# Kernel tuning notes

Hardware: AMD Instinct MI355X
Metric: run time of the kernel (lower is better)

Reference implementation:

```python
import jax, jax.numpy as jnp
import numpy as np

EMBED_DIM = 1024
NUM_HEADS = 16
HEAD_DIM = EMBED_DIM // NUM_HEADS
B, S = 4, 1024
EPS = 1e-5
NEG = -1e9


def layer_norm(h, gamma, beta):
    mu = jnp.mean(h, axis=-1, keepdims=True)
    var = jnp.mean(jnp.square(h - mu), axis=-1, keepdims=True)
    return (h - mu) * jax.lax.rsqrt(var + EPS) * gamma + beta


def setup_inputs() -> dict:
    key = jax.random.key(0)
    ks = jax.random.split(key, 8)
    scale = 1.0 / np.sqrt(EMBED_DIM)
    x = jax.random.normal(ks[0], (B, S, EMBED_DIM), dtype=jnp.float32)
    mask = jax.random.randint(ks[1], (B, S, S), 0, 2).astype(jnp.bool_)
    Wq = jax.random.uniform(ks[2], (EMBED_DIM, EMBED_DIM), jnp.float32, -scale, scale)
    bq = jax.random.uniform(ks[3], (EMBED_DIM,), jnp.float32, -scale, scale)
    Wk = jax.random.uniform(ks[4], (EMBED_DIM, EMBED_DIM), jnp.float32, -scale, scale)
    bk = jax.random.uniform(ks[5], (EMBED_DIM,), jnp.float32, -scale, scale)
    gq = jnp.ones((EMBED_DIM,), jnp.float32)
    bq_n = jnp.zeros((EMBED_DIM,), jnp.float32)
    gk = jnp.ones((EMBED_DIM,), jnp.float32)
    bk_n = jnp.zeros((EMBED_DIM,), jnp.float32)
    return {"x": x, "mask": mask, "Wq": Wq, "bq": bq, "Wk": Wk, "bk": bk,
            "gq": gq, "bq_n": bq_n, "gk": gk, "bk_n": bk_n}


def reference(x, mask, Wq, bq, Wk, bk, gq, bq_n, gk, bk_n):
    b, s, _ = x.shape
    # proj -> LayerNorm -> ReLU, split heads: [B,S,H,D]
    Q = jax.nn.relu(layer_norm(x @ Wq + bq, gq, bq_n)).reshape(b, s, NUM_HEADS, HEAD_DIM)
    K = jax.nn.relu(layer_norm(x @ Wk + bk, gk, bk_n)).reshape(b, s, NUM_HEADS, HEAD_DIM)
    # scores [B,H,S,S]
    scores = jnp.einsum('bqhd,bkhd->bhqk', Q, K) / np.sqrt(HEAD_DIM).astype(np.float32)
    # symmetric masking: mask applied along keys, then (via transpose trick) along queries
    m = (mask | jnp.swapaxes(mask, -1, -2))[:, None, :, :]
    scores = jnp.where(m, NEG, scores)
    attn = jax.nn.softmax(scores, axis=-1)
    return attn.mean(axis=1)  # [B,S,S]
```

## Files before the change

### kernel.cpp

```cpp
#include <hip/hip_runtime.h>
#include <hip/hip_bf16.h>

#define B_ 4
#define S_ 1024
#define E_ 1024
#define H_ 16
#define D_ 64

typedef __attribute__((ext_vector_type(8))) short short8;
typedef __attribute__((ext_vector_type(4))) float f32x4;

static __device__ __forceinline__ unsigned short f2bf(float x) {
  unsigned int u = __float_as_uint(x);
  unsigned int r = u + 0x7fffu + ((u >> 16) & 1u);
  return (unsigned short)(r >> 16);
}
static __device__ __forceinline__ float bf2f(unsigned short b) {
  return __uint_as_float((unsigned int)b << 16);
}

#define GL2LDS16(g, l)                                                            \
  __builtin_amdgcn_global_load_lds(                                               \
      (const __attribute__((address_space(1))) unsigned int*)(g),                 \
      (__attribute__((address_space(3))) unsigned int*)(l), 16, 0, 0)

__global__ __launch_bounds__(256) void mask_sym_kernel(const int* __restrict__ mask,
                                                       unsigned char* __restrict__ msym) {
  const int blk = blockIdx.x;
  const int b = blk >> 10;
  const int rest = blk & 1023;
  const int i0 = (rest >> 5) << 5;
  const int j0 = (rest & 31) << 5;
  __shared__ int T[32][33];
  const int tid = threadIdx.x;
  const int ii = tid >> 3;
  const int jj4 = (tid & 7) << 2;
  const size_t bO = (size_t)b * S_ * S_;
  const int4 m2 = *(const int4*)&mask[bO + (size_t)(j0 + ii) * S_ + i0 + jj4];
  T[ii][jj4 + 0] = m2.x; T[ii][jj4 + 1] = m2.y; T[ii][jj4 + 2] = m2.z; T[ii][jj4 + 3] = m2.w;
  __syncthreads();
  const int4 m1 = *(const int4*)&mask[bO + (size_t)(i0 + ii) * S_ + j0 + jj4];
  uchar4 o;
  o.x = ((m1.x != 0) || (T[jj4 + 0][ii] != 0)) ? 1 : 0;
  o.y = ((m1.y != 0) || (T[jj4 + 1][ii] != 0)) ? 1 : 0;
  o.z = ((m1.z != 0) || (T[jj4 + 2][ii] != 0)) ? 1 : 0;
  o.w = ((m1.w != 0) || (T[jj4 + 3][ii] != 0)) ? 1 : 0;
  *(uchar4*)&msym[bO + (size_t)(i0 + ii) * S_ + j0 + jj4] = o;
}

__global__ __launch_bounds__(256) void cvt_x_kernel(const float* __restrict__ x,
                                                    unsigned short* __restrict__ o) {
  const size_t i = ((size_t)blockIdx.x * 256 + threadIdx.x) * 8;
  const float4 a = *(const float4*)(x + i);
  const float4 b = *(const float4*)(x + i + 4);
  const ushort4 p0 = {f2bf(a.x), f2bf(a.y), f2bf(a.z), f2bf(a.w)};
  const ushort4 p1 = {f2bf(b.x), f2bf(b.y), f2bf(b.z), f2bf(b.w)};
  *(ushort4*)(o + i) = p0;
  *(ushort4*)(o + i + 4) = p1;
}

__global__ __launch_bounds__(256) void wt_kernel(const float* __restrict__ Wq,
                                                 const float* __restrict__ Wk,
                                                 unsigned short* __restrict__ Wt) {
  const int blk = blockIdx.x;
  const int mat = blk >> 10;
  const int kt = (blk >> 5) & 31, ntb = blk & 31;
  const float* W = mat ? Wk : Wq;
  __shared__ unsigned short T[32][36];
  const int tid = threadIdx.x;
  const int r = tid >> 3, c4 = (tid & 7) << 2;
  const float4 v = *(const float4*)&W[(size_t)(kt * 32 + r) * 1024 + ntb * 32 + c4];
  T[r][c4 + 0] = f2bf(v.x); T[r][c4 + 1] = f2bf(v.y);
  T[r][c4 + 2] = f2bf(v.z); T[r][c4 + 3] = f2bf(v.w);
  __syncthreads();
  const ushort4 o = {T[c4 + 0][r], T[c4 + 1][r], T[c4 + 2][r], T[c4 + 3][r]};
  *(ushort4*)&Wt[(size_t)(mat * 1024 + ntb * 32 + r) * 1024 + kt * 32 + c4] = o;
}

__global__ __launch_bounds__(256) void gemm_mfma_kernel(const unsigned short* __restrict__ Abf,
                                                        const unsigned short* __restrict__ Wt,
                                                        unsigned short* __restrict__ P,
                                                        int nstride) {
  __shared__ __align__(16) unsigned short As[128 * 32];
  __shared__ __align__(16) unsigned short Bs[128 * 32];
  const int tid = threadIdx.x;
  const int m0 = (blockIdx.x & 31) << 7;
  const int n0 = (blockIdx.x >> 5) << 7;
  const int wave = tid >> 6, lane = tid & 63;
  const int ln15 = lane & 15, rg = lane >> 4;
  const int wm = (wave & 1) << 6;
  const int wn = (wave >> 1) << 6;
  const int sr = tid >> 2;
  const int sc = (tid & 3) << 3;
  const unsigned short* gA = Abf + (size_t)(m0 + sr) * 1024 + sc;
  const unsigned short* gB = Wt + (size_t)(n0 + sr) * 1024 + sc;
  unsigned short* lA = As + tid * 8;
  unsigned short* lB = Bs + tid * 8;
  f32x4 acc[4][4];
#pragma unroll
  for (int i = 0; i < 4; ++i)
#pragma unroll
    for (int j = 0; j < 4; ++j) acc[i][j] = (f32x4){0.0f, 0.0f, 0.0f, 0.0f};

  const unsigned short* pa = As + (wm + ln15) * 32 + rg * 8;
  const unsigned short* pb = Bs + (wn + ln15) * 32 + rg * 8;
  for (int k0 = 0; k0 < E_; k0 += 32) {
    GL2LDS16(gA + k0, lA);
    GL2LDS16(gA + k0 + (size_t)64 * 1024, lA + 2048);
    GL2LDS16(gB + k0, lB);
    GL2LDS16(gB + k0 + (size_t)64 * 1024, lB + 2048);
    __syncthreads();
    short8 af[4], bfr[4];
#pragma unroll
    for (int i = 0; i < 4; ++i) af[i] = *(const short8*)(pa + i * 16 * 32);
#pragma unroll
    for (int j = 0; j < 4; ++j) bfr[j] = *(const short8*)(pb + j * 16 * 32);
#pragma unroll
    for (int i = 0; i < 4; ++i)
#pragma unroll
      for (int j = 0; j < 4; ++j)
        acc[i][j] = __builtin_amdgcn_mfma_f32_16x16x32_bf16(af[i], bfr[j], acc[i][j], 0, 0, 0);
    __syncthreads();
  }
#pragma unroll
  for (int i = 0; i < 4; ++i)
#pragma unroll
    for (int j = 0; j < 4; ++j)
#pragma unroll
      for (int r = 0; r < 4; ++r) {
        const int row = m0 + wm + i * 16 + rg * 4 + r;
        const int col = n0 + wn + j * 16 + ln15;
        P[(size_t)row * nstride + col] = f2bf(acc[i][j][r]);
      }
}

__global__ __launch_bounds__(256) void ln_relu_bf_kernel(const unsigned short* __restrict__ P,
                                                         int rowstride, int coloff,
                                                         const float* __restrict__ bias,
                                                         const float* __restrict__ gamma,
                                                         const float* __restrict__ beta,
                                                         unsigned short* __restrict__ obf) {
  const int row = blockIdx.x;
  const int b = row >> 10, s = row & 1023;
  const unsigned short* p = P + (size_t)row * rowstride + coloff;
  const int tid = threadIdx.x;
  const ushort4 pv = *(const ushort4*)(p + tid * 4);
  float4 v = {bf2f(pv.x), bf2f(pv.y), bf2f(pv.z), bf2f(pv.w)};
  const float4 bb = ((const float4*)bias)[tid];
  v.x += bb.x; v.y += bb.y; v.z += bb.z; v.w += bb.w;
  float sum = v.x + v.y + v.z + v.w;
  float s2 = v.x * v.x + v.y * v.y + v.z * v.z + v.w * v.w;
#pragma unroll
  for (int off = 32; off >= 1; off >>= 1) {
    sum += __shfl_xor(sum, off);
    s2 += __shfl_xor(s2, off);
  }
  __shared__ float red[2][4];
  const int wave = tid >> 6, lane = tid & 63;
  if (lane == 0) { red[0][wave] = sum; red[1][wave] = s2; }
  __syncthreads();
  sum = red[0][0] + red[0][1] + red[0][2] + red[0][3];
  s2 = red[1][0] + red[1][1] + red[1][2] + red[1][3];
  const float mu = sum * (1.0f / E_);
  const float var = s2 * (1.0f / E_) - mu * mu;
  const float r = rsqrtf(var + 1e-5f);
  const float4 g = ((const float4*)gamma)[tid];
  const float4 bt = ((const float4*)beta)[tid];
  const float o0 = fmaxf((v.x - mu) * r * g.x + bt.x, 0.0f);
  const float o1 = fmaxf((v.y - mu) * r * g.y + bt.y, 0.0f);
  const float o2 = fmaxf((v.z - mu) * r * g.z + bt.z, 0.0f);
  const float o3 = fmaxf((v.w - mu) * r * g.w + bt.w, 0.0f);
  const int h = tid >> 4;
  const int d = (tid & 15) << 2;
  const ushort4 ob = {f2bf(o0), f2bf(o1), f2bf(o2), f2bf(o3)};
  *(ushort4*)&obf[((size_t)(b * H_ + h) * S_ + s) * D_ + d] = ob;
}

__global__ __launch_bounds__(1024, 4) void attn4_kernel(const unsigned short* __restrict__ Qbf,
                                                        const unsigned short* __restrict__ Kbf,
                                                        const unsigned char* __restrict__ msym,
                                                        float* __restrict__ out) {
  __shared__ __align__(16) float outAcc[16][1028];
  __shared__ __align__(16) float l_lds[16][4][16];
  __shared__ __align__(16) float linv_lds[4][16];
  const int tid = threadIdx.x;
  const int wave = tid >> 6, lane = tid & 63;
  const int ln15 = lane & 15, rg = lane >> 4;
  const int blk = blockIdx.x;
  const int b = blk & 3;
  const int q0 = (blk >> 2) << 4;
  const int k0 = wave << 6;

  unsigned int mbits = 0;
#pragma unroll
  for (int jt = 0; jt < 4; ++jt)
#pragma unroll
    for (int r = 0; r < 4; ++r)
      mbits |= (msym[((size_t)b * S_ + q0 + rg * 4 + r) * S_ + k0 + jt * 16 + ln15] ? 1u : 0u)
               << (jt * 4 + r);

  const size_t bbase = (size_t)b * H_ * S_ * D_;
  const size_t qoff = (size_t)(q0 + ln15) * D_ + rg * 8;
  const size_t koff = (size_t)(k0 + ln15) * D_ + rg * 8;

  float o[4][4] = {};
#pragma unroll 1
  for (int c = 0; c < 4; ++c) {
    unsigned int epack[4][4][2];
#pragma unroll
    for (int hh = 0; hh < 4; ++hh) {
      const size_t hbase = bbase + (size_t)(c * 4 + hh) * S_ * D_;
      const unsigned short* qp = Qbf + hbase + qoff;
      const short8 a0 = *(const short8*)qp;
      const short8 a1 = *(const short8*)(qp + 32);
      const unsigned short* kp = Kbf + hbase + koff;
      float la[4] = {0.0f, 0.0f, 0.0f, 0.0f};
#pragma unroll
      for (int jt = 0; jt < 4; ++jt) {
        const unsigned short* kpj = kp + (size_t)jt * (16 * D_);
        const short8 b0 = *(const short8*)kpj;
        const short8 b1 = *(const short8*)(kpj + 32);
        f32x4 cc = {0.0f, 0.0f, 0.0f, 0.0f};
        cc = __builtin_amdgcn_mfma_f32_16x16x32_bf16(a0, b0, cc, 0, 0, 0);
        cc = __builtin_amdgcn_mfma_f32_16x16x32_bf16(a1, b1, cc, 0, 0, 0);
        float e[4];
#pragma unroll
        for (int r = 0; r < 4; ++r) {
          const float s = fminf(cc[r] * 0.125f, 80.0f);
          e[r] = ((mbits >> (jt * 4 + r)) & 1u) ? 0.0f : __expf(s);
          la[r] += e[r];
        }
        epack[hh][jt][0] = (unsigned)f2bf(e[0]) | ((unsigned)f2bf(e[1]) << 16);
        epack[hh][jt][1] = (unsigned)f2bf(e[2]) | ((unsigned)f2bf(e[3]) << 16);
      }
#pragma unroll
      for (int r = 0; r < 4; ++r) {
        float lv = la[r];
        lv += __shfl_xor(lv, 1);
        lv += __shfl_xor(lv, 2);
        lv += __shfl_xor(lv, 4);
        lv += __shfl_xor(lv, 8);
        la[r] = lv;
      }
      if (ln15 == 0) {
        const float4 lw = {la[0], la[1], la[2], la[3]};
        *(float4*)&l_lds[wave][hh][rg * 4] = lw;
      }
    }
    __syncthreads();
    if (tid < 64) {
      const int hh = tid >> 4, q = tid & 15;
      float s = 0.0f;
#pragma unroll
      for (int w = 0; w < 16; ++w) s += l_lds[w][hh][q];
      linv_lds[hh][q] = 0.0625f / s;
    }
    __syncthreads();
#pragma unroll
    for (int hh = 0; hh < 4; ++hh) {
      const float4 li4 = *(const float4*)&linv_lds[hh][rg * 4];
#pragma unroll
      for (int jt = 0; jt < 4; ++jt) {
        const unsigned u0 = epack[hh][jt][0], u1 = epack[hh][jt][1];
        o[jt][0] += __uint_as_float(u0 << 16) * li4.x;
        o[jt][1] += __uint_as_float(u0 & 0xFFFF0000u) * li4.y;
        o[jt][2] += __uint_as_float(u1 << 16) * li4.z;
        o[jt][3] += __uint_as_float(u1 & 0xFFFF0000u) * li4.w;
      }
    }
  }
#pragma unroll
  for (int jt = 0; jt < 4; ++jt)
#pragma unroll
    for (int r = 0; r < 4; ++r)
      outAcc[rg * 4 + r][k0 + jt * 16 + ln15] = o[jt][r];
  __syncthreads();
  {
    const int row = tid >> 6, c0 = (tid & 63) << 4;
    float* dst = out + ((size_t)b * S_ + q0 + row) * S_ + c0;
    const float* srcA = &outAcc[row][c0];
#pragma unroll
    for (int i = 0; i < 4; ++i)
      *(float4*)(dst + i * 4) = *(const float4*)(srcA + i * 4);
  }
}

extern "C" void kernel_launch(void* const* d_in, const int* in_sizes, int n_in,
                              void* d_out, int out_size, void* d_ws, size_t ws_size,
                              hipStream_t stream) {
  const float* x = (const float*)d_in[0];
  const int* mask = (const int*)d_in[1];
  const float* Wq = (const float*)d_in[2];
  const float* bq = (const float*)d_in[3];
  const float* Wk = (const float*)d_in[4];
  const float* bk = (const float*)d_in[5];
  const float* gq = (const float*)d_in[6];
  const float* bq_n = (const float*)d_in[7];
  const float* gk = (const float*)d_in[8];
  const float* bk_n = (const float*)d_in[9];
  float* out = (float*)d_out;

  char* ws = (char*)d_ws;
  const size_t MB = 1024 * 1024;

  if (ws_size >= 40 * MB) {
    unsigned short* P2 = (unsigned short*)ws;
    unsigned short* xbf = (unsigned short*)(ws + 16 * MB);
    unsigned short* Kbf = (unsigned short*)(ws + 16 * MB);
    unsigned short* Wt = (unsigned short*)(ws + 24 * MB);
    unsigned short* Qbf = (unsigned short*)(ws + 28 * MB);
    unsigned char* msym = (unsigned char*)(ws + 36 * MB);

    mask_sym_kernel<<<4096, 256, 0, stream>>>(mask, msym);
    cvt_x_kernel<<<2048, 256, 0, stream>>>(x, xbf);
    wt_kernel<<<2048, 256, 0, stream>>>(Wq, Wk, Wt);
    gemm_mfma_kernel<<<512, 256, 0, stream>>>(xbf, Wt, P2, 2048);
    ln_relu_bf_kernel<<<4096, 256, 0, stream>>>(P2, 2048, 0, bq, gq, bq_n, Qbf);
    ln_relu_bf_kernel<<<4096, 256, 0, stream>>>(P2, 2048, 1024, bk, gk, bk_n, Kbf);
    attn4_kernel<<<256, 1024, 0, stream>>>(Qbf, Kbf, msym, out);
  } else {
    unsigned short* P = (unsigned short*)ws;
    unsigned short* xbf = (unsigned short*)(ws + 8 * MB);
    unsigned short* Kbf = (unsigned short*)(ws + 8 * MB);
    unsigned short* Wt = (unsigned short*)(ws + 16 * MB);
    unsigned short* Qbf = (unsigned short*)(ws + 20 * MB);
    unsigned char* msym = (unsigned char*)(ws + 28 * MB);

    mask_sym_kernel<<<4096, 256, 0, stream>>>(mask, msym);
    cvt_x_kernel<<<2048, 256, 0, stream>>>(x, xbf);
    wt_kernel<<<2048, 256, 0, stream>>>(Wq, Wk, Wt);
    gemm_mfma_kernel<<<256, 256, 0, stream>>>(xbf, Wt, P, 1024);
    ln_relu_bf_kernel<<<4096, 256, 0, stream>>>(P, 1024, 0, bq, gq, bq_n, Qbf);
    gemm_mfma_kernel<<<256, 256, 0, stream>>>(xbf, Wt + (size_t)1024 * 1024, P, 1024);
    ln_relu_bf_kernel<<<4096, 256, 0, stream>>>(P, 1024, 0, bk, gk, bk_n, Kbf);
    attn4_kernel<<<256, 1024, 0, stream>>>(Qbf, Kbf, msym, out);
  }
}
```

Measured before the change: 227.8 us.

## Stage Q/K tiles in swizzled LDS with double-buffered K prefetch; merge prep kernels

The attention kernel now loads all 16 heads of the block's Q rows into swizzled LDS once. It streams K for each head and key quarter through a double-buffered LDS tile with register prefetch, so each wave reads MFMA operands from LDS instead of scattered global loads. The softmax normalisation moves to one pass per head, and outputs are written directly rather than staged through a large LDS accumulator. Separately, the mask symmetrisation, x conversion and weight transpose kernels are merged into one launch by block-index ranges. The new schedule adds a __syncthreads per key step and uses more LDS per block, which may limit occupancy.

```diff
diff --git a/kernel.cpp b/kernel.cpp
--- a/kernel.cpp
+++ b/kernel.cpp
@@ -24,57 +24,57 @@
       (const __attribute__((address_space(1))) unsigned int*)(g),                 \
       (__attribute__((address_space(3))) unsigned int*)(l), 16, 0, 0)
 
-__global__ __launch_bounds__(256) void mask_sym_kernel(const int* __restrict__ mask,
-                                                       unsigned char* __restrict__ msym) {
+__global__ __launch_bounds__(256) void prep_kernel(const int* __restrict__ mask,
+                                                   const float* __restrict__ x,
+                                                   const float* __restrict__ Wq,
+                                                   const float* __restrict__ Wk,
+                                                   unsigned char* __restrict__ msym,
+                                                   unsigned short* __restrict__ xbf,
+                                                   unsigned short* __restrict__ Wt) {
+  __shared__ __align__(16) char u_lds[32 * 33 * 4];
   const int blk = blockIdx.x;
-  const int b = blk >> 10;
-  const int rest = blk & 1023;
-  const int i0 = (rest >> 5) << 5;
-  const int j0 = (rest & 31) << 5;
-  __shared__ int T[32][33];
   const int tid = threadIdx.x;
-  const int ii = tid >> 3;
-  const int jj4 = (tid & 7) << 2;
-  const size_t bO = (size_t)b * S_ * S_;
-  const int4 m2 = *(const int4*)&mask[bO + (size_t)(j0 + ii) * S_ + i0 + jj4];
-  T[ii][jj4 + 0] = m2.x; T[ii][jj4 + 1] = m2.y; T[ii][jj4 + 2] = m2.z; T[ii][jj4 + 3] = m2.w;
-  __syncthreads();
-  const int4 m1 = *(const int4*)&mask[bO + (size_t)(i0 + ii) * S_ + j0 + jj4];
-  uchar4 o;
-  o.x = ((m1.x != 0) || (T[jj4 + 0][ii] != 0)) ? 1 : 0;
-  o.y = ((m1.y != 0) || (T[jj4 + 1][ii] != 0)) ? 1 : 0;
-  o.z = ((m1.z != 0) || (T[jj4 + 2][ii] != 0)) ? 1 : 0;
-  o.w = ((m1.w != 0) || (T[jj4 + 3][ii] != 0)) ? 1 : 0;
-  *(uchar4*)&msym[bO + (size_t)(i0 + ii) * S_ + j0 + jj4] = o;
-}
-
-__global__ __launch_bounds__(256) void cvt_x_kernel(const float* __restrict__ x,
-                                                    unsigned short* __restrict__ o) {
-  const size_t i = ((size_t)blockIdx.x * 256 + threadIdx.x) * 8;
-  const float4 a = *(const float4*)(x + i);
-  const float4 b = *(const float4*)(x + i + 4);
-  const ushort4 p0 = {f2bf(a.x), f2bf(a.y), f2bf(a.z), f2bf(a.w)};
-  const ushort4 p1 = {f2bf(b.x), f2bf(b.y), f2bf(b.z), f2bf(b.w)};
-  *(ushort4*)(o + i) = p0;
-  *(ushort4*)(o + i + 4) = p1;
-}
-
-__global__ __launch_bounds__(256) void wt_kernel(const float* __restrict__ Wq,
-                                                 const float* __restrict__ Wk,
-                                                 unsigned short* __restrict__ Wt) {
-  const int blk = blockIdx.x;
-  const int mat = blk >> 10;
-  const int kt = (blk >> 5) & 31, ntb = blk & 31;
-  const float* W = mat ? Wk : Wq;
-  __shared__ unsigned short T[32][36];
-  const int tid = threadIdx.x;
-  const int r = tid >> 3, c4 = (tid & 7) << 2;
-  const float4 v = *(const float4*)&W[(size_t)(kt * 32 + r) * 1024 + ntb * 32 + c4];
-  T[r][c4 + 0] = f2bf(v.x); T[r][c4 + 1] = f2bf(v.y);
-  T[r][c4 + 2] = f2bf(v.z); T[r][c4 + 3] = f2bf(v.w);
-  __syncthreads();
-  const ushort4 o = {T[c4 + 0][r], T[c4 + 1][r], T[c4 + 2][r], T[c4 + 3][r]};
-  *(ushort4*)&Wt[(size_t)(mat * 1024 + ntb * 32 + r) * 1024 + kt * 32 + c4] = o;
+  if (blk < 4096) {
+    int (*T)[33] = (int(*)[33])u_lds;
+    const int b = blk >> 10;
+    const int rest = blk & 1023;
+    const int i0 = (rest >> 5) << 5;
+    const int j0 = (rest & 31) << 5;
+    const int ii = tid >> 3;
+    const int jj4 = (tid & 7) << 2;
+    const size_t bO = (size_t)b * S_ * S_;
+    const int4 m2 = *(const int4*)&mask[bO + (size_t)(j0 + ii) * S_ + i0 + jj4];
+    T[ii][jj4 + 0] = m2.x; T[ii][jj4 + 1] = m2.y; T[ii][jj4 + 2] = m2.z; T[ii][jj4 + 3] = m2.w;
+    __syncthreads();
+    const int4 m1 = *(const int4*)&mask[bO + (size_t)(i0 + ii) * S_ + j0 + jj4];
+    uchar4 o;
+    o.x = ((m1.x != 0) || (T[jj4 + 0][ii] != 0)) ? 1 : 0;
+    o.y = ((m1.y != 0) || (T[jj4 + 1][ii] != 0)) ? 1 : 0;
+    o.z = ((m1.z != 0) || (T[jj4 + 2][ii] != 0)) ? 1 : 0;
+    o.w = ((m1.w != 0) || (T[jj4 + 3][ii] != 0)) ? 1 : 0;
+    *(uchar4*)&msym[bO + (size_t)(i0 + ii) * S_ + j0 + jj4] = o;
+  } else if (blk < 6144) {
+    const size_t i = ((size_t)(blk - 4096) * 256 + tid) * 8;
+    const float4 a = *(const float4*)(x + i);
+    const float4 b = *(const float4*)(x + i + 4);
+    const ushort4 p0 = {f2bf(a.x), f2bf(a.y), f2bf(a.z), f2bf(a.w)};
+    const ushort4 p1 = {f2bf(b.x), f2bf(b.y), f2bf(b.z), f2bf(b.w)};
+    *(ushort4*)(xbf + i) = p0;
+    *(ushort4*)(xbf + i + 4) = p1;
+  } else {
+    unsigned short (*T2)[36] = (unsigned short(*)[36])u_lds;
+    const int wblk = blk - 6144;
+    const int mat = wblk >> 10;
+    const int kt = (wblk >> 5) & 31, ntb = wblk & 31;
+    const float* W = mat ? Wk : Wq;
+    const int r = tid >> 3, c4 = (tid & 7) << 2;
+    const float4 v = *(const float4*)&W[(size_t)(kt * 32 + r) * 1024 + ntb * 32 + c4];
+    T2[r][c4 + 0] = f2bf(v.x); T2[r][c4 + 1] = f2bf(v.y);
+    T2[r][c4 + 2] = f2bf(v.z); T2[r][c4 + 3] = f2bf(v.w);
+    __syncthreads();
+    const ushort4 o = {T2[c4 + 0][r], T2[c4 + 1][r], T2[c4 + 2][r], T2[c4 + 3][r]};
+    *(ushort4*)&Wt[(size_t)(mat * 1024 + ntb * 32 + r) * 1024 + kt * 32 + c4] = o;
+  }
 }
 
 __global__ __launch_bounds__(256) void gemm_mfma_kernel(const unsigned short* __restrict__ Abf,
@@ -176,113 +176,130 @@
   *(ushort4*)&obf[((size_t)(b * H_ + h) * S_ + s) * D_ + d] = ob;
 }
 
-__global__ __launch_bounds__(1024, 4) void attn4_kernel(const unsigned short* __restrict__ Qbf,
+__global__ __launch_bounds__(1024, 4) void attn5_kernel(const unsigned short* __restrict__ Qbf,
                                                         const unsigned short* __restrict__ Kbf,
                                                         const unsigned char* __restrict__ msym,
                                                         float* __restrict__ out) {
-  __shared__ __align__(16) float outAcc[16][1028];
-  __shared__ __align__(16) float l_lds[16][4][16];
-  __shared__ __align__(16) float linv_lds[4][16];
+  __shared__ __align__(16) unsigned short Qs[256 * 64];
+  __shared__ __align__(16) unsigned short Ks[2][256 * 64];
+  __shared__ __align__(16) float l_lds[16][16];
+  __shared__ __align__(16) float linv[16];
   const int tid = threadIdx.x;
   const int wave = tid >> 6, lane = tid & 63;
   const int ln15 = lane & 15, rg = lane >> 4;
-  const int blk = blockIdx.x;
-  const int b = blk & 3;
-  const int q0 = (blk >> 2) << 4;
-  const int k0 = wave << 6;
-
+  const int b = blockIdx.x & 3;
+  const int q0 = (blockIdx.x >> 2) << 4;
+
+  const unsigned short* Kb = Kbf + (size_t)b * H_ * S_ * D_;
+
+  {
+    const int rho = tid >> 3, p = tid & 7;
+    const int c = p ^ (rho & 7);
+    const int rho2 = rho + 128;
+    const int c2 = p ^ (rho2 & 7);
+    const uint4 v0 = *(const uint4*)(Qbf + ((size_t)(b * H_ + (rho >> 4)) * S_ + q0 + (rho & 15)) * D_ + c * 8);
+    const uint4 v1 = *(const uint4*)(Qbf + ((size_t)(b * H_ + (rho2 >> 4)) * S_ + q0 + (rho2 & 15)) * D_ + c2 * 8);
+    *(uint4*)&Qs[rho * 64 + p * 8] = v0;
+    *(uint4*)&Qs[rho2 * 64 + p * 8] = v1;
+  }
   unsigned int mbits = 0;
 #pragma unroll
-  for (int jt = 0; jt < 4; ++jt)
+  for (int qt = 0; qt < 4; ++qt)
 #pragma unroll
     for (int r = 0; r < 4; ++r)
-      mbits |= (msym[((size_t)b * S_ + q0 + rg * 4 + r) * S_ + k0 + jt * 16 + ln15] ? 1u : 0u)
-               << (jt * 4 + r);
-
-  const size_t bbase = (size_t)b * H_ * S_ * D_;
-  const size_t qoff = (size_t)(q0 + ln15) * D_ + rg * 8;
-  const size_t koff = (size_t)(k0 + ln15) * D_ + rg * 8;
+      mbits |= (msym[((size_t)b * S_ + q0 + rg * 4 + r) * S_ + qt * 256 + wave * 16 + ln15] ? 1u : 0u)
+               << (qt * 4 + r);
+
+  const int krow = tid >> 3, kp = tid & 7;
+  const int kcc = kp ^ (krow & 7);
+  {
+    const unsigned short* src = Kb + (size_t)krow * D_ + kcc * 8;
+    const uint4 p0 = *(const uint4*)src;
+    const uint4 p1 = *(const uint4*)(src + 128 * D_);
+    *(uint4*)&Ks[0][krow * 64 + kp * 8] = p0;
+    *(uint4*)&Ks[0][(krow + 128) * 64 + kp * 8] = p1;
+  }
+  __syncthreads();
+
+  const int pfrag = (rg ^ (ln15 & 7)) * 8;
+  const unsigned short* QsW = Qs + ln15 * 64;
+  const unsigned short* KsW0 = Ks[0] + (wave * 16 + ln15) * 64;
+  const unsigned short* KsW1 = Ks[1] + (wave * 16 + ln15) * 64;
 
   float o[4][4] = {};
+  unsigned int epack[4][2];
+  uint4 pf0, pf1;
+
 #pragma unroll 1
-  for (int c = 0; c < 4; ++c) {
-    unsigned int epack[4][4][2];
-#pragma unroll
-    for (int hh = 0; hh < 4; ++hh) {
-      const size_t hbase = bbase + (size_t)(c * 4 + hh) * S_ * D_;
-      const unsigned short* qp = Qbf + hbase + qoff;
-      const short8 a0 = *(const short8*)qp;
-      const short8 a1 = *(const short8*)(qp + 32);
-      const unsigned short* kp = Kbf + hbase + koff;
-      float la[4] = {0.0f, 0.0f, 0.0f, 0.0f};
-#pragma unroll
-      for (int jt = 0; jt < 4; ++jt) {
-        const unsigned short* kpj = kp + (size_t)jt * (16 * D_);
-        const short8 b0 = *(const short8*)kpj;
-        const short8 b1 = *(const short8*)(kpj + 32);
-        f32x4 cc = {0.0f, 0.0f, 0.0f, 0.0f};
-        cc = __builtin_amdgcn_mfma_f32_16x16x32_bf16(a0, b0, cc, 0, 0, 0);
-        cc = __builtin_amdgcn_mfma_f32_16x16x32_bf16(a1, b1, cc, 0, 0, 0);
-        float e[4];
-#pragma unroll
-        for (int r = 0; r < 4; ++r) {
-          const float s = fminf(cc[r] * 0.125f, 80.0f);
-          e[r] = ((mbits >> (jt * 4 + r)) & 1u) ? 0.0f : __expf(s);
-          la[r] += e[r];
-        }
-        epack[hh][jt][0] = (unsigned)f2bf(e[0]) | ((unsigned)f2bf(e[1]) << 16);
-        epack[hh][jt][1] = (unsigned)f2bf(e[2]) | ((unsigned)f2bf(e[3]) << 16);
+  for (int h = 0; h < 16; ++h) {
+    const unsigned short* qrow = QsW + h * 16 * 64;
+    const short8 a0 = *(const short8*)(qrow + pfrag);
+    const short8 a1 = *(const short8*)(qrow + (pfrag ^ 32));
+    float la[4] = {0.0f, 0.0f, 0.0f, 0.0f};
+#pragma unroll
+    for (int qt = 0; qt < 4; ++qt) {
+      const int s = h * 4 + qt;
+      if (s < 63) {
+        const int s1 = s + 1;
+        const unsigned short* src =
+            Kb + ((size_t)(s1 >> 2) * S_ + ((s1 & 3) << 8) + krow) * D_ + kcc * 8;
+        pf0 = *(const uint4*)src;
+        pf1 = *(const uint4*)(src + 128 * D_);
       }
+      const unsigned short* kw = (qt & 1) ? KsW1 : KsW0;
+      const short8 b0 = *(const short8*)(kw + pfrag);
+      const short8 b1 = *(const short8*)(kw + (pfrag ^ 32));
+      f32x4 cc = {0.0f, 0.0f, 0.0f, 0.0f};
+      cc = __builtin_amdgcn_mfma_f32_16x16x32_bf16(a0, b0, cc, 0, 0, 0);
+      cc = __builtin_amdgcn_mfma_f32_16x16x32_bf16(a1, b1, cc, 0, 0, 0);
+      float e[4];
 #pragma unroll
       for (int r = 0; r < 4; ++r) {
-        float lv = la[r];
-        lv += __shfl_xor(lv, 1);
-        lv += __shfl_xor(lv, 2);
-        lv += __shfl_xor(lv, 4);
-        lv += __shfl_xor(lv, 8);
-        la[r] = lv;
+        const float sv = fminf(cc[r] * 0.125f, 80.0f);
+        e[r] = ((mbits >> (qt * 4 + r)) & 1u) ? 0.0f : __expf(sv);
+        la[r] += e[r];
       }
-      if (ln15 == 0) {
-        const float4 lw = {la[0], la[1], la[2], la[3]};
-        *(float4*)&l_lds[wave][hh][rg * 4] = lw;
+      epack[qt][0] = (unsigned)f2bf(e[0]) | ((unsigned)f2bf(e[1]) << 16);
+      epack[qt][1] = (unsigned)f2bf(e[2]) | ((unsigned)f2bf(e[3]) << 16);
+      if (s < 63) {
+        unsigned short* dst = (qt & 1) ? Ks[0] : Ks[1];
+        *(uint4*)&dst[krow * 64 + kp * 8] = pf0;
+        *(uint4*)&dst[(krow + 128) * 64 + kp * 8] = pf1;
       }
+      if (qt < 3) __syncthreads();
     }
-    __syncthreads();
-    if (tid < 64) {
-      const int hh = tid >> 4, q = tid & 15;
-      float s = 0.0f;
-#pragma unroll
-      for (int w = 0; w < 16; ++w) s += l_lds[w][hh][q];
-      linv_lds[hh][q] = 0.0625f / s;
+#pragma unroll
+    for (int r = 0; r < 4; ++r) {
+      float lv = la[r];
+      lv += __shfl_xor(lv, 1);
+      lv += __shfl_xor(lv, 2);
+      lv += __shfl_xor(lv, 4);
+      lv += __shfl_xor(lv, 8);
+      la[r] = lv;
     }
-    __syncthreads();
-#pragma unroll
-    for (int hh = 0; hh < 4; ++hh) {
-      const float4 li4 = *(const float4*)&linv_lds[hh][rg * 4];
-#pragma unroll
-      for (int jt = 0; jt < 4; ++jt) {
-        const unsigned u0 = epack[hh][jt][0], u1 = epack[hh][jt][1];
-        o[jt][0] += __uint_as_float(u0 << 16) * li4.x;
-        o[jt][1] += __uint_as_float(u0 & 0xFFFF0000u) * li4.y;
-        o[jt][2] += __uint_as_float(u1 << 16) * li4.z;
-        o[jt][3] += __uint_as_float(u1 & 0xFFFF0000u) * li4.w;
-      }
+    if (ln15 == 0) *(float4*)&l_lds[wave][rg * 4] = (float4){la[0], la[1], la[2], la[3]};
+    __syncthreads();
+    if (tid < 16) {
+      float ssum = 0.0f;
+#pragma unroll
+      for (int w = 0; w < 16; ++w) ssum += l_lds[w][tid];
+      linv[tid] = 0.0625f / ssum;
     }
-  }
-#pragma unroll
-  for (int jt = 0; jt < 4; ++jt)
+    __syncthreads();
+    const float4 li4 = *(const float4*)&linv[rg * 4];
+#pragma unroll
+    for (int qt = 0; qt < 4; ++qt) {
+      o[qt][0] += __uint_as_float(epack[qt][0] << 16) * li4.x;
+      o[qt][1] += __uint_as_float(epack[qt][0] & 0xFFFF0000u) * li4.y;
+      o[qt][2] += __uint_as_float(epack[qt][1] << 16) * li4.z;
+      o[qt][3] += __uint_as_float(epack[qt][1] & 0xFFFF0000u) * li4.w;
+    }
+  }
+#pragma unroll
+  for (int qt = 0; qt < 4; ++qt)
 #pragma unroll
     for (int r = 0; r < 4; ++r)
-      outAcc[rg * 4 + r][k0 + jt * 16 + ln15] = o[jt][r];
-  __syncthreads();
-  {
-    const int row = tid >> 6, c0 = (tid & 63) << 4;
-    float* dst = out + ((size_t)b * S_ + q0 + row) * S_ + c0;
-    const float* srcA = &outAcc[row][c0];
-#pragma unroll
-    for (int i = 0; i < 4; ++i)
-      *(float4*)(dst + i * 4) = *(const float4*)(srcA + i * 4);
-  }
+      out[((size_t)b * S_ + q0 + rg * 4 + r) * S_ + qt * 256 + wave * 16 + ln15] = o[qt][r];
 }
 
 extern "C" void kernel_launch(void* const* d_in, const int* in_sizes, int n_in,
@@ -311,13 +328,11 @@
     unsigned short* Qbf = (unsigned short*)(ws + 28 * MB);
     unsigned char* msym = (unsigned char*)(ws + 36 * MB);
 
-    mask_sym_kernel<<<4096, 256, 0, stream>>>(mask, msym);
-    cvt_x_kernel<<<2048, 256, 0, stream>>>(x, xbf);
-    wt_kernel<<<2048, 256, 0, stream>>>(Wq, Wk, Wt);
+    prep_kernel<<<8192, 256, 0, stream>>>(mask, x, Wq, Wk, msym, xbf, Wt);
     gemm_mfma_kernel<<<512, 256, 0, stream>>>(xbf, Wt, P2, 2048);
     ln_relu_bf_kernel<<<4096, 256, 0, stream>>>(P2, 2048, 0, bq, gq, bq_n, Qbf);
     ln_relu_bf_kernel<<<4096, 256, 0, stream>>>(P2, 2048, 1024, bk, gk, bk_n, Kbf);
-    attn4_kernel<<<256, 1024, 0, stream>>>(Qbf, Kbf, msym, out);
+    attn5_kernel<<<256, 1024, 0, stream>>>(Qbf, Kbf, msym, out);
   } else {
     unsigned short* P = (unsigned short*)ws;
     unsigned short* xbf = (unsigned short*)(ws + 8 * MB);
@@ -326,13 +341,11 @@
     unsigned short* Qbf = (unsigned short*)(ws + 20 * MB);
     unsigned char* msym = (unsigned char*)(ws + 28 * MB);
 
-    mask_sym_kernel<<<4096, 256, 0, stream>>>(mask, msym);
-    cvt_x_kernel<<<2048, 256, 0, stream>>>(x, xbf);
-    wt_kernel<<<2048, 256, 0, stream>>>(Wq, Wk, Wt);
+    prep_kernel<<<8192, 256, 0, stream>>>(mask, x, Wq, Wk, msym, xbf, Wt);
     gemm_mfma_kernel<<<256, 256, 0, stream>>>(xbf, Wt, P, 1024);
     ln_relu_bf_kernel<<<4096, 256, 0, stream>>>(P, 1024, 0, bq, gq, bq_n, Qbf);
     gemm_mfma_kernel<<<256, 256, 0, stream>>>(xbf, Wt + (size_t)1024 * 1024, P, 1024);
     ln_relu_bf_kernel<<<4096, 256, 0, stream>>>(P, 1024, 0, bk, gk, bk_n, Kbf);
-    attn4_kernel<<<256, 1024, 0, stream>>>(Qbf, Kbf, msym, out);
-  }
-}
+    attn5_kernel<<<256, 1024, 0, stream>>>(Qbf, Kbf, msym, out);
+  }
+}
```

Measured after the change: 201.6 us. 1.13x faster.
